# Kernel tuning notes

Hardware: AMD Instinct MI355X
Metric: run time of the kernel (lower is better)

The kernel has to match this reference:

```python
import jax, jax.numpy as jnp
import numpy as np
from math import factorial

N_OBJS = 23

def _f(n):
    return float(factorial(n))

def wigner_d(l, beta):
    """Wigner small-d matrix d^l_{m',m}(beta); shape [2l+1, 2l+1]; m', m in -l..l."""
    mv = np.arange(-l, l + 1)
    cb, sb = np.cos(beta / 2.0), np.sin(beta / 2.0)
    d = np.zeros((2 * l + 1, 2 * l + 1))
    for i, mp in enumerate(mv):
        for j, m in enumerate(mv):
            pref = np.sqrt(_f(l + mp) * _f(l - mp) * _f(l + m) * _f(l - m))
            acc = 0.0
            for s in range(max(0, m - mp), min(l + m, l - mp) + 1):
                acc += ((-1.0) ** (mp - m + s)
                        / (_f(l + m - s) * _f(s) * _f(mp - m + s) * _f(l - mp - s))
                        * cb ** (2 * l + m - mp - 2 * s) * sb ** (mp - m + 2 * s))
            d[i, j] = pref * acc
    return d

def dh_betas(b):
    return np.pi * (2 * np.arange(2 * b) + 1) / (4 * b)

def quad_weights(b):
    """Driscoll-Healy quadrature weights over the 2b beta samples."""
    j = np.arange(2 * b)[:, None]
    k = np.arange(b)[None, :]
    s = (np.sin((2 * j + 1) * (2 * k + 1) * np.pi / (4 * b)) / (2 * k + 1)).sum(1)
    return (2.0 / b) * np.sin(np.pi * (2 * np.arange(2 * b) + 1) / (4 * b)) * s

def s2_fft(x, b_in, nl):
    # x: [N, f, 2b(beta), 2b(alpha)] real -> list over l of [N, f, 2l+1] complex
    xf = jnp.fft.fft(x, axis=-1)
    betas, qw = dh_betas(b_in), quad_weights(b_in)
    out = []
    for l in range(nl):
        dl = np.stack([wigner_d(l, bb)[:, l] for bb in betas])  # [2b, 2l+1] = d^l_{m,0}
        w = jnp.asarray((dl * qw[:, None]).astype(np.complex64))
        idx = np.arange(-l, l + 1) % (2 * b_in)
        out.append(jnp.einsum('nfbm,bm->nfm', xf[..., idx], w))
    return out

def so3_fft(x, b_in, nl):
    # x: [N, f, 2b(beta), 2b(alpha), 2b(gamma)] -> list over l of [N, f, 2l+1, 2l+1]
    xf = jnp.fft.fft2(x, axes=(-2, -1)) / float((2 * b_in) ** 2)
    betas, qw = dh_betas(b_in), quad_weights(b_in)
    out = []
    for l in range(nl):
        d = (np.stack([wigner_d(l, bb) for bb in betas]) * qw[:, None, None]).astype(np.complex64)
        idx = np.arange(-l, l + 1) % (2 * b_in)
        xm = xf[:, :, :, idx[:, None], idx[None, :]]  # [N,f,2b,2l+1,2l+1]
        out.append(jnp.einsum('kmn,afkmn->afmn', jnp.asarray(d), xm))
    return out

def so3_ifft(Z, b):
    # Z: list over l of [N, f, 2l+1, 2l+1] -> real [N, f, 2b, 2b, 2b]
    N, f = Z[0].shape[:2]
    betas = dh_betas(b)
    S = jnp.zeros((N, f, 2 * b, 2 * b, 2 * b), dtype=jnp.complex64)
    for l, Zl in enumerate(Z):
        d = (np.stack([wigner_d(l, bb) for bb in betas]) * (2 * l + 1)).astype(np.complex64)
        T = jnp.einsum('kmn,afmn->afkmn', jnp.asarray(d), Zl)
        idx = np.arange(-l, l + 1) % (2 * b)
        S = S.at[:, :, :, idx[:, None], idx[None, :]].add(T)
    return (jnp.fft.ifft2(S, axes=(-2, -1)) * float((2 * b) ** 2)).real

def s2_rft(kern, nl, alphas, betas):
    # kern: [f_in, f_out, G] real -> list over l of [f_in, f_out, 2l+1] complex
    out = []
    for l in range(nl):
        m = np.arange(-l, l + 1)
        d = np.stack([wigner_d(l, bb)[:, l] for bb in betas])  # [G, 2l+1]
        basis = (d * np.exp(-1j * m[None, :] * alphas[:, None])).astype(np.complex64)
        out.append(jnp.einsum('iog,gm->iom', kern, jnp.asarray(basis)))
    return out

def so3_rft(kern, nl, alphas, betas, gammas):
    out = []
    for l in range(nl):
        m = np.arange(-l, l + 1)
        d = np.stack([wigner_d(l, bb) for bb in betas])  # [G, 2l+1, 2l+1]
        basis = (np.exp(-1j * m[None, :, None] * alphas[:, None, None]) * d
                 * np.exp(-1j * m[None, None, :] * gammas[:, None, None])).astype(np.complex64)
        out.append(jnp.einsum('iog,gmn->iomn', kern, jnp.asarray(basis)))
    return out

def s2_near_identity_grid(n_alpha, n_beta, max_beta=np.pi / 8):
    beta = np.arange(1, n_beta + 1) * max_beta / n_beta
    alpha = np.linspace(0, 2 * np.pi, n_alpha, endpoint=False)
    B, A = np.meshgrid(beta, alpha, indexing='ij')
    return A.ravel(), B.ravel()

def so3_near_identity_grid(n_alpha, n_beta, n_gamma, max_beta=np.pi / 8, max_gamma=np.pi / 8):
    beta = np.arange(1, n_beta + 1) * max_beta / n_beta
    alpha = np.linspace(0, 2 * np.pi, n_alpha, endpoint=False)
    gamma = np.linspace(-max_gamma, max_gamma, n_gamma)
    B, A, G = np.meshgrid(beta, alpha, gamma, indexing='ij')
    return A.ravel(), B.ravel(), G.ravel()

def bn3d(x, w, b, eps=1e-5):
    mu = x.mean(axis=(0, 2, 3, 4), keepdims=True)
    var = x.var(axis=(0, 2, 3, 4), keepdims=True)
    return (x - mu) * jax.lax.rsqrt(var + eps) * w[None, :, None, None, None] + b[None, :, None, None, None]

def bn1d(x, w, b, eps=1e-5):
    mu = x.mean(0)
    var = x.var(0)
    return (x - mu) * jax.lax.rsqrt(var + eps) * w + b

def s2_block(x, kern, bias, bnw, bnb, b_in, b_out):
    X = s2_fft(x, b_in, b_out)
    a, be = s2_near_identity_grid(2 * b_in, 2)
    scale = float(1.0 / np.sqrt(kern.shape[2] * kern.shape[0]))
    Y = s2_rft(kern * scale, b_out, a, be)
    Z = [jnp.einsum('aim,ion->aomn', X[l], jnp.conj(Y[l])) for l in range(b_out)]
    y = so3_ifft(Z, b_out) + bias[None, :, None, None, None]
    return jax.nn.relu(bn3d(y, bnw, bnb))

def so3_block(x, kern, bias, bnw, bnb, b_in, b_out):
    X = so3_fft(x, b_in, b_out)
    a, be, g = so3_near_identity_grid(2 * b_in, 2, 2)
    scale = float(1.0 / np.sqrt(kern.shape[2] * kern.shape[0]))
    Y = so3_rft(kern * scale, b_out, a, be, g)
    Z = [jnp.einsum('aimk,ionk->aomn', X[l], jnp.conj(Y[l])) for l in range(b_out)]
    y = so3_ifft(Z, b_out) + bias[None, :, None, None, None]
    return jax.nn.relu(bn3d(y, bnw, bnb))

def so3_integrate(x):
    b = x.shape[-1] // 2
    w = jnp.asarray(quad_weights(b).astype(np.float32))
    return (x.mean(axis=(-2, -1)) * w).sum(-1)  # weighted beta sum, mean over alpha/gamma

def forward(x, atom_types, k0, c0, g0, d0, k1, c1, g1, d1, k2, c2, g2, d2, k3, c3, g3, d3,
            W1, b1, gw1, gb1, W2, b2, gw2, gb2, W3, b3, gw3, gb3, W4, b4):
    B, n_atoms = x.shape[0], x.shape[1]
    mask = (atom_types > 0).astype(x.dtype)[:, :, None]  # [B, 23, 1]
    h = x.reshape(B * n_atoms, x.shape[2], x.shape[3], x.shape[4])
    h = s2_block(h, k0, c0, g0, d0, 10, 8)
    h = so3_block(h, k1, c1, g1, d1, 8, 6)
    h = so3_block(h, k2, c2, g2, d2, 6, 4)
    h = so3_block(h, k3, c3, g3, d3, 4, 2)
    h = so3_integrate(h)  # [B*23, 64]
    h = jax.nn.relu(bn1d(h @ W1 + b1, gw1, gb1))
    h = jax.nn.relu(bn1d(h @ W2 + b2, gw2, gb2))
    h = (h.reshape(B, N_OBJS, -1) * mask).sum(1)
    h = jax.nn.relu(bn1d(h @ W3 + b3, gw3, gb3))
    return h @ W4 + b4

def setup_inputs():
    key = jax.random.key(0)
    ks = jax.random.split(key, 12)
    B = 64
    return {
        'x': jax.random.normal(ks[0], (B, 23, 5, 20, 20), jnp.float32),
        'atom_types': jax.random.randint(ks[1], (B, 23), 0, 10),
        'k0': jax.random.normal(ks[2], (5, 8, 40), jnp.float32),
        'c0': jnp.zeros((8,), jnp.float32), 'g0': jnp.ones((8,), jnp.float32), 'd0': jnp.zeros((8,), jnp.float32),
        'k1': jax.random.normal(ks[3], (8, 16, 64), jnp.float32),
        'c1': jnp.zeros((16,), jnp.float32), 'g1': jnp.ones((16,), jnp.float32), 'd1': jnp.zeros((16,), jnp.float32),
        'k2': jax.random.normal(ks[4], (16, 32, 48), jnp.float32),
        'c2': jnp.zeros((32,), jnp.float32), 'g2': jnp.ones((32,), jnp.float32), 'd2': jnp.zeros((32,), jnp.float32),
        'k3': jax.random.normal(ks[5], (32, 64, 32), jnp.float32),
        'c3': jnp.zeros((64,), jnp.float32), 'g3': jnp.ones((64,), jnp.float32), 'd3': jnp.zeros((64,), jnp.float32),
        'W1': jax.random.normal(ks[6], (64, 256), jnp.float32) * 0.125,
        'b1': jnp.zeros((256,), jnp.float32), 'gw1': jnp.ones((256,), jnp.float32), 'gb1': jnp.zeros((256,), jnp.float32),
        'W2': jax.random.normal(ks[7], (256, 64), jnp.float32) * 0.0625,
        'b2': jnp.zeros((64,), jnp.float32), 'gw2': jnp.ones((64,), jnp.float32), 'gb2': jnp.zeros((64,), jnp.float32),
        'W3': jax.random.normal(ks[8], (64, 512), jnp.float32) * 0.125,
        'b3': jnp.zeros((512,), jnp.float32), 'gw3': jnp.ones((512,), jnp.float32), 'gb3': jnp.zeros((512,), jnp.float32),
        'W4': jax.random.normal(ks[9], (512, 1), jnp.float32) * 0.044,
        'b4': jnp.zeros((1,), jnp.float32),
    }

def reference(x, atom_types, k0, c0, g0, d0, k1, c1, g1, d1, k2, c2, g2, d2, k3, c3, g3, d3,
              W1, b1, gw1, gb1, W2, b2, gw2, gb2, W3, b3, gw3, gb3, W4, b4):
    return forward(x, atom_types, k0, c0, g0, d0, k1, c1, g1, d1, k2, c2, g2, d2, k3, c3, g3, d3,
                   W1, b1, gw1, gb1, W2, b2, gw2, gb2, W3, b3, gw3, gb3, W4, b4)
```

## Files before the change

kernel.cpp:

```cpp
#include <hip/hip_runtime.h>
#include <cmath>


#define NSAMP 1472
#define PI_D 3.14159265358979323846

constexpr int cBI[4] = {10, 8, 6, 4};
constexpr int cBO[4] = {8, 6, 4, 2};
constexpr int cFI[4] = {5, 8, 16, 32};
constexpr int cFO[4] = {8, 16, 32, 64};
constexpr int cG [4] = {40, 64, 48, 32};
constexpr int cSQ[4] = {680, 286, 84, 10};

__host__ __device__ constexpr int zof(int l) { return (4*l*l*l - l)/3; }

constexpr size_t al64(size_t x){ return (x + 63) & ~(size_t)63; }
constexpr size_t OFS_WF0 = 0;
constexpr size_t OFS_WF1 = al64(OFS_WF0 + 20*64);
constexpr size_t OFS_WF2 = al64(OFS_WF1 + 16*286);
constexpr size_t OFS_WF3 = al64(OFS_WF2 + 12*84);
constexpr size_t OFS_WI0 = al64(OFS_WF3 + 8*10);
constexpr size_t OFS_WI1 = al64(OFS_WI0 + 16*680);
constexpr size_t OFS_WI2 = al64(OFS_WI1 + 12*286);
constexpr size_t OFS_WI3 = al64(OFS_WI2 + 8*84);
// ... 205 lines not shown
            float kv = kr[g];
            float2 b = Bc[bbase + g*w + n];
            re += kv*b.x; im += kv*b.y;
        }
        YC[ybase + t] = make_float2(re, im);
    }
}

__global__ __launch_bounds__(256)
void k_fwd_s2(const float* __restrict__ x, float2* __restrict__ X,
              const float2* __restrict__ Ff, const float* __restrict__ Wf){
    __shared__ float xv[400];
    __shared__ float2 xf[300];
    int tid = threadIdx.x;
    const float* src = x + (size_t)blockIdx.x * 400;
    for (int t = tid; t < 400; t += 256) xv[t] = src[t];
    __syncthreads();
    for (int t = tid; t < 300; t += 256){
        int mi = t % 15, b = t / 15;
        float re = 0.f, im = 0.f;
        for (int al = 0; al < 20; ++al){
            float v = xv[b*20 + al];
            float2 e = Ff[al*15 + mi];
            re += v*e.x; im += v*e.y;
        }
        xf[t] = make_float2(re, im);
    }
    __syncthreads();
    float2* dst = X + (size_t)blockIdx.x * 64;
    int base = 0, lo = 0;
    for (int l = 0; l < 8; ++l){
        int w = 2*l+1;
        for (int t = tid; t < w; t += 256){
            int mi = t - l + 7;
            float re = 0.f, im = 0.f;
            for (int b = 0; b < 20; ++b){
                float wv = Wf[base + b*w + t];
                float2 v = xf[b*15 + mi];
                re += wv*v.x; im += wv*v.y;
            }
            dst[lo + t] = make_float2(re, im);
        }
        base += 20*w; lo += w;
    }
}

template<int T, int L>
__device__ inline float2 mixE(const float2* __restrict__ xs, const float2* __restrict__ Y,
                              int o, int m, int n){
    constexpr int w = 2*L+1;
    constexpr int FI = cFI[T], FO = cFO[T], SQ = cSQ[T];
    float re = 0.f, im = 0.f;
    if constexpr (T == 0){
        const float2* yb = Y + 40*L*L + o*w + n;
        #pragma unroll
        for (int i = 0; i < FI; ++i){
            float2 x = xs[i*64 + L*L + m];
            float2 y = yb[i*8*w];
            re += x.x*y.x - x.y*y.y;
            im += x.x*y.y + x.y*y.x;
        }
    } else {
        const float2* yb = Y + FI*FO*zof(L) + (size_t)o*w + n;
        for (int i = 0; i < FI; ++i){
            const float2* xp = xs + i*SQ + zof(L) + m*w;
            const float2* yp = yb + (size_t)i*w*FO*w;
            #pragma unroll
            for (int k = 0; k < w; ++k){
                float2 x = xp[k];
                float2 y = yp[(size_t)k*FO*w];
                re += x.x*y.x - x.y*y.y;
                im += x.x*y.y + x.y*y.x;
            }
        }
    }
    return make_float2(re, im);
}

template<int T, int OB>
__global__ __launch_bounds__(256)
void k_mix(const float2* __restrict__ Xin, const float2* __restrict__ Y,
           const float* __restrict__ G, const float* __restrict__ hT,
           float2* __restrict__ Z, float2* __restrict__ bnp)
{
    constexpr int FI = cFI[T], FO = cFO[T], NL = cBO[T];
    constexpr int NF = 2*NL-1, OFF = NL-1, SQ = cSQ[T], P = 2*NL;
    constexpr int XPER = (T==0) ? 64 : SQ;
    __shared__ float2 xs[FI*XPER];
    __shared__ float2 zs[OB*SQ];
    const int tid = threadIdx.x;
    constexpr int NOB = FO/OB;
    const int o0 = (blockIdx.x % NOB)*OB;
    const int a  = blockIdx.x / NOB;
    for (int t = tid; t < FI*XPER; t += 256) xs[t] = Xin[(size_t)a*FI*XPER + t];
    __syncthreads();
    float2* Zg = Z + ((size_t)a*FO + o0)*SQ;
    for (int e = tid; e < OB*SQ; e += 256){
        int osub = e / SQ, rem = e % SQ;
        int o = o0 + osub;
        int l = 0, r2 = rem;
        while (r2 >= (2*l+1)*(2*l+1)){ r2 -= (2*l+1)*(2*l+1); ++l; }
        int w = 2*l+1;
        int m = r2 / w, n = r2 % w;
        float2 val = make_float2(0.f, 0.f);
        switch(l){
            case 0: val = mixE<T,0>(xs, Y, o, m, n); break;
            case 1: if constexpr (1 < NL) val = mixE<T,1>(xs, Y, o, m, n); break;
            case 2: if constexpr (2 < NL) val = mixE<T,2>(xs, Y, o, m, n); break;
            case 3: if constexpr (3 < NL) val = mixE<T,3>(xs, Y, o, m, n); break;
            case 4: if constexpr (4 < NL) val = mixE<T,4>(xs, Y, o, m, n); break;
            case 5: if constexpr (5 < NL) val = mixE<T,5>(xs, Y, o, m, n); break;
            case 6: if constexpr (6 < NL) val = mixE<T,6>(xs, Y, o, m, n); break;
            case 7: if constexpr (7 < NL) val = mixE<T,7>(xs, Y, o, m, n); break;
        }
        zs[e] = val;
        Zg[(size_t)osub*SQ + rem] = val;
    }
    __syncthreads();
    const int wave = tid >> 6, lane = tid & 63;
    for (int osub = wave; osub < OB; osub += 4){
        const float2* zp = zs + osub*SQ;
        float pq = 0.f, p0 = 0.f;
        for (int e = lane; e < NF*NF; e += 64){
            int mi = e / NF, ni = e % NF;
            int mm = mi - OFF, nn = ni - OFF;
            int am = mm<0?-mm:mm, an = nn<0?-nn:nn;
            float zr[8], zi[8];
            #pragma unroll
            for (int l = 0; l < NL; ++l){
                bool ok = (l >= am) && (l >= an);
                int idx = ok ? (zof(l) + (mm+l)*(2*l+1) + (nn+l)) : 0;
                float2 zv = zp[idx];
                zr[l] = ok ? zv.x : 0.f;
                zi[l] = ok ? zv.y : 0.f;
            }
            #pragma unroll
            for (int l = 0; l < NL; ++l){
                #pragma unroll
                for (int l2 = 0; l2 < NL; ++l2){
                    float g = G[(l*NL + l2)*NF*NF + e];
                    pq += g*(zr[l]*zr[l2] + zi[l]*zi[l2]);
                }
            }
        }
        if (lane < NL){
            int l = lane;
            p0 = hT[l] * zp[zof(l) + l*(2*l+1) + l].x;
        }
        for (int s = 32; s > 0; s >>= 1){ p0 += __shfl_down(p0, s); pq += __shfl_down(pq, s); }
        if (lane == 0) bnp[(size_t)(o0+osub)*NSAMP + a] = make_float2((float)(P*P)*p0, (float)(P*P)*pq);
    }
}

template<int T, int OB, int CH>
__global__ __launch_bounds__(256)
void k_finv(const float2* __restrict__ Z, const float* __restrict__ Wi, const float2* __restrict__ Fi,
            const float2* __restrict__ Ff, const float* __restrict__ Wf,
            const float* __restrict__ st, const float* __restrict__ gam, const float* __restrict__ bet,
            float2* __restrict__ Xout)
{
    constexpr int FO = cFO[T], NL = cBO[T];
    constexpr int P = 2*NL, NF = 2*NL-1, OFF = NL-1, SQ = cSQ[T];
    constexpr int Tn = T+1;
    constexpr int NLo = cBO[Tn], NFo = 2*NLo-1, OFFo = NLo-1, SQo = cSQ[Tn];
    constexpr float invP2 = 1.0f/(float)(P*P);
    constexpr int szZS = OB*SQ*8;
    constexpr int offS = szZS;
    constexpr int szS  = OB*CH*NF*NF*8;
    constexpr int offT1 = offS + szS;
    constexpr int szT1 = OB*CH*P*NF*8;
    constexpr int szT1B = OB*P*P*NFo*8;
    constexpr int endT1 = offT1 + szT1;
    constexpr int offD = (endT1 > szT1B) ? endT1 : szT1B;
    constexpr int szXV = OB*P*P*P*4;
    constexpr int szSP = OB*P*NFo*NFo*8;
    static_assert(szSP <= szXV, "spec overlay exceeds xv");
    constexpr int LDSZ = offD + szXV;
    __shared__ __align__(16) char smem[LDSZ];
    float2* zs  = (float2*)smem;
    float2* Ssh = (float2*)(smem + offS);
    float2* t1s = (float2*)(smem + offT1);
    float*  xv  = (float*)(smem + offD);

    const int tid = threadIdx.x;
    constexpr int NOB = FO/OB;
    const int o0 = (blockIdx.x % NOB)*OB;
    const int a  = blockIdx.x / NOB;

    for (int t = tid; t < OB*SQ; t += 256) zs[t] = Z[((size_t)a*FO + o0)*SQ + t];
    __syncthreads();

    for (int c0 = 0; c0 < P; c0 += CH){
        for (int t = tid; t < OB*CH*NF*NF; t += 256){
            int ni = t % NF, mi = (t/NF) % NF, kk = (t/(NF*NF)) % CH, osub = t/(NF*NF*CH);
            int k = c0 + kk;
            int mm = mi - OFF, nn = ni - OFF;
            int am = mm < 0 ? -mm : mm, an = nn < 0 ? -nn : nn;
            int l0 = am > an ? am : an;
            const float2* zp = zs + osub*SQ;
            float re = 0.f, im = 0.f;
            int zb = zof(l0);
            for (int l = l0; l < NL; ++l){
                int w = 2*l+1, szl = w*w;
                int rc = (mm + l)*w + (nn + l);
                float wv = Wi[P*zb + k*szl + rc];
                float2 zv = zp[zb + rc];
                re += wv*zv.x; im += wv*zv.y;
                zb += szl;
            }
            Ssh[t] = make_float2(re, im);
        }
        __syncthreads();
        for (int t = tid; t < OB*CH*P*NF; t += 256){
            int ni = t % NF, al = (t/NF) % P, kk = (t/(NF*P)) % CH, osub = t/(NF*P*CH);
            const float2* sb = &Ssh[(osub*CH + kk)*NF*NF];
            float re = 0.f, im = 0.f;
            for (int mi = 0; mi < NF; ++mi){
                float2 s = sb[mi*NF + ni];
                float2 e = Fi[al*NF + mi];
                re += s.x*e.x - s.y*e.y;
                im += s.x*e.y + s.y*e.x;
            }
            t1s[t] = make_float2(re, im);
        }
        __syncthreads();
        for (int t = tid; t < OB*CH*P*P; t += 256){
            int ga = t % P, al = (t/P) % P, kk = (t/(P*P)) % CH, osub = t/(P*P*CH);
            const float2* tb = &t1s[((osub*CH + kk)*P + al)*NF];
            float re = 0.f;
            for (int ni = 0; ni < NF; ++ni){
                float2 v = tb[ni];
                float2 e = Fi[ga*NF + ni];
                re += v.x*e.x - v.y*e.y;
            }
            xv[(osub*P + c0 + kk)*P*P + al*P + ga] = re;
        }
        __syncthreads();
    }

    for (int t = tid; t < OB*P*P*P; t += 256){
        int o = o0 + t/(P*P*P);
        float v = xv[t];
        xv[t] = fmaxf(0.f, (v - st[2*o])*st[2*o+1]*gam[o] + bet[o]);
    }
    __syncthreads();

    float2* t1b = (float2*)smem;
    for (int t = tid; t < OB*P*P*NFo; t += 256){
        int n = t % NFo, kj = (t/NFo) % (P*P), osub = t/(NFo*P*P);
        const float* row = &xv[osub*P*P*P + kj*P];
        float re = 0.f, im = 0.f;
        for (int j = 0; j < P; ++j){
            float v = row[j];
            float2 e = Ff[j*NFo + n];
            re += v*e.x; im += v*e.y;
        }
        t1b[t] = make_float2(re, im);
    }
    __syncthreads();
    float2* spec = (float2*)(smem + offD);
    for (int t = tid; t < OB*P*NFo*NFo; t += 256){
        int n = t % NFo, m = (t/NFo) % NFo, k = (t/(NFo*NFo)) % P, osub = t/(NFo*NFo*P);
        const float2* tb = t1b + osub*P*P*NFo;
        float re = 0.f, im = 0.f;
        for (int j = 0; j < P; ++j){
            float2 v = tb[(k*P + j)*NFo + n];
            float2 e = Ff[j*NFo + m];
            re += v.x*e.x - v.y*e.y;
            im += v.x*e.y + v.y*e.x;
        }
        spec[t] = make_float2(re*invP2, im*invP2);
    }
    __syncthreads();
    for (int t = tid; t < OB*SQo; t += 256){
        int osub = t / SQo, e2 = t % SQo;
        int l = 0, rem = e2;
        while (rem >= (2*l+1)*(2*l+1)){ rem -= (2*l+1)*(2*l+1); ++l; }
        int w = 2*l+1;
        int i2 = rem / w, j2 = rem % w;
        int mi = i2 - l + OFFo, ni = j2 - l + OFFo;
        const float2* sp = spec + osub*P*NFo*NFo;
        float re = 0.f, im = 0.f;
        for (int k = 0; k < P; ++k){
            float wv = Wf[P*zof(l) + k*(w*w) + rem];
            float2 v = sp[(k*NFo + mi)*NFo + ni];
            re += wv*v.x; im += wv*v.y;
        }
        Xout[((size_t)a*FO + o0 + osub)*SQo + e2] = make_float2(re, im);
    }
}

template<int T, int MODE, int OB>
__global__ __launch_bounds__(256)
void k_trans(const float2* __restrict__ Xin, const float2* __restrict__ Y,
             const float* __restrict__ Wi, const float2* __restrict__ Fi,
             const float2* __restrict__ Ff, const float* __restrict__ Wf,
             const float* __restrict__ st, const float* __restrict__ gam, const float* __restrict__ bet,
             float2* __restrict__ Xout, float2* __restrict__ bnp)
{
    constexpr int FI = cFI[T], FO = cFO[T], NL = cBO[T];
    constexpr int P = 2*NL, NF = 2*NL-1, OFF = NL-1, SQ = cSQ[T];
    constexpr int XPER = (T==0) ? 64 : SQ;
    constexpr int Tn = (T < 3) ? T + 1 : 3;
    constexpr int NLo = cBO[Tn], NFo = 2*NLo-1, OFFo = NLo-1, SQo = cSQ[Tn];
    constexpr int CH = (T==0) ? 4 : ((T==1) ? 6 : P);
    constexpr float invP2 = 1.0f/(float)(P*P);

    constexpr int szXS  = FI*XPER*8;
    constexpr int offZS = szXS;
    constexpr int szZS  = OB*SQ*8;
    constexpr int offB  = offZS + szZS;
    constexpr int offS  = offB;
    constexpr int szS   = OB*CH*NF*NF*8;
    constexpr int offT1 = offS + szS;
    constexpr int szT1  = OB*CH*P*NF*8;
    constexpr int offD  = offT1 + szT1;
    constexpr int szXV  = OB*P*P*P*4;
    constexpr int LDSZ = MODE ? (offD + szXV) : (offB + 64);

    __shared__ __align__(16) char smem[LDSZ];
    float2* xs = (float2*)(smem);
    float2* zs = (float2*)(smem + offZS);

    const int tid = threadIdx.x;
    constexpr int NOB = FO/OB;
    const int o0 = (blockIdx.x % NOB) * OB;
    const int a  = blockIdx.x / NOB;

    for (int t = tid; t < FI*XPER; t += 256) xs[t] = Xin[(size_t)a*FI*XPER + t];
    __syncthreads();

    for (int e = tid; e < OB*SQ; e += 256){
        int osub = e / SQ, rem = e % SQ;
        int o = o0 + osub;
        int l = 0;
        while (rem >= (2*l+1)*(2*l+1)){ rem -= (2*l+1)*(2*l+1); ++l; }
        int w = 2*l+1;
        int m = rem / w, n = rem % w;
        float re = 0.f, im = 0.f;
        if constexpr (T == 0){
            const float2* yb = Y + 40*l*l + o*w + n;
            for (int i = 0; i < FI; ++i){
                float2 xv2 = xs[i*64 + l*l + m];
                float2 y = yb[i*8*w];
                re += xv2.x*y.x - xv2.y*y.y;
                im += xv2.x*y.y + xv2.y*y.x;
            }
        } else {
            const float2* yb = Y + FI*FO*zof(l);
            for (int i = 0; i < FI; ++i){
                const float2* xp = &xs[i*SQ + zof(l) + m*w];
                const float2* yp = yb + ((size_t)i*w*FO + o)*w + n;
                for (int k = 0; k < w; ++k){
                    float2 xv2 = xp[k];
                    float2 y = yp[(size_t)k*FO*w];
                    re += xv2.x*y.x - xv2.y*y.y;
                    im += xv2.x*y.y + xv2.y*y.x;
                }
            }
        }
        zs[e] = make_float2(re, im);
    }
    __syncthreads();

    if constexpr (MODE == 0){
        float* wred = (float*)(smem + offB);
        if constexpr (OB == 1){
            float acc0 = 0.f, accQ = 0.f;
            for (int t = tid; t < P*NF*NF; t += 256){
                int ni = t % NF, mi = (t/NF) % NF, k = t/(NF*NF);
                int mm = mi - OFF, nn = ni - OFF;
                int am = mm < 0 ? -mm : mm, an = nn < 0 ? -nn : nn;
                int l0 = am > an ? am : an;
                float re = 0.f, im = 0.f;
                int zb = zof(l0);
                for (int l = l0; l < NL; ++l){
                    int w = 2*l+1, szl = w*w;
                    int rc = (mm + l)*w + (nn + l);
                    float wv = Wi[P*zb + k*szl + rc];
                    float2 zv = zs[zb + rc];
                    re += wv*zv.x; im += wv*zv.y;
                    zb += szl;
                }
                accQ += re*re + im*im;
                if (mm == 0 && nn == 0) acc0 += re;
            }
            for (int s = 32; s > 0; s >>= 1){ acc0 += __shfl_down(acc0, s); accQ += __shfl_down(accQ, s); }
            if ((tid & 63) == 0){ wred[tid>>6] = acc0; wred[4 + (tid>>6)] = accQ; }
            __syncthreads();
            if (tid == 0){
                float a0 = 0.f, a1 = 0.f;
                for (int u = 0; u < 4; ++u){ a0 += wred[u]; a1 += wred[4+u]; }
                bnp[(size_t)o0*NSAMP + a] = make_float2((float)(P*P)*a0, (float)(P*P)*a1);
            }
        } else {
            static_assert(OB == 1 || OB == 4, "stats path expects OB==1 or 4");
            const int wave = tid >> 6, lane = tid & 63;
            const float2* zp = zs + wave*SQ;
            float acc0 = 0.f, accQ = 0.f;
            for (int t = lane; t < P*NF*NF; t += 64){
                int ni = t % NF, mi = (t/NF) % NF, k = t/(NF*NF);
                int mm = mi - OFF, nn = ni - OFF;
                int am = mm < 0 ? -mm : mm, an = nn < 0 ? -nn : nn;
                int l0 = am > an ? am : an;
                float re = 0.f, im = 0.f;
                int zb = zof(l0);
                for (int l = l0; l < NL; ++l){
                    int w = 2*l+1, szl = w*w;
                    int rc = (mm + l)*w + (nn + l);
                    float wv = Wi[P*zb + k*szl + rc];
                    float2 zv = zp[zb + rc];
                    re += wv*zv.x; im += wv*zv.y;
                    zb += szl;
                }
                accQ += re*re + im*im;
                if (mm == 0 && nn == 0) acc0 += re;
            }
            for (int s = 32; s > 0; s >>= 1){ acc0 += __shfl_down(acc0, s); accQ += __shfl_down(accQ, s); }
            if (lane == 0) bnp[(size_t)(o0+wave)*NSAMP + a] = make_float2((float)(P*P)*acc0, (float)(P*P)*accQ);
        }
    } else {
        float2* Ssh = (float2*)(smem + offS);
        float2* t1s = (float2*)(smem + offT1);
        float*  xv  = (float*)(smem + offD);

        for (int c0 = 0; c0 < P; c0 += CH){
            for (int t = tid; t < OB*CH*NF*NF; t += 256){
                int ni = t % NF, mi = (t/NF) % NF, kk = (t/(NF*NF)) % CH, osub = t/(NF*NF*CH);
                int k = c0 + kk;
                int mm = mi - OFF, nn = ni - OFF;
                int am = mm < 0 ? -mm : mm, an = nn < 0 ? -nn : nn;
                int l0 = am > an ? am : an;
                const float2* zp = zs + osub*SQ;
                float re = 0.f, im = 0.f;
                int zb = zof(l0);
                for (int l = l0; l < NL; ++l){
                    int w = 2*l+1, szl = w*w;
                    int rc = (mm + l)*w + (nn + l);
                    float wv = Wi[P*zb + k*szl + rc];
                    float2 zv = zp[zb + rc];
                    re += wv*zv.x; im += wv*zv.y;
// ... 209 lines not shown
    pre1[(size_t)r*256 + tid] = acc;
}

__global__ __launch_bounds__(256)
void k_colstats(const float* __restrict__ x, float* __restrict__ st, int nrow, int ncol){
    int c = blockIdx.x, tid = threadIdx.x;
    double s = 0.0, q = 0.0;
    for (int r = tid; r < nrow; r += 256){
        float v = x[(size_t)r*ncol + c];
        s += v; q += (double)v*(double)v;
    }
    for (int o = 32; o > 0; o >>= 1){ s += __shfl_down(s, o); q += __shfl_down(q, o); }
    __shared__ double rs_[4], rq_[4];
    if ((tid & 63) == 0){ rs_[tid>>6] = s; rq_[tid>>6] = q; }
    __syncthreads();
    if (tid == 0){
        double S = 0.0, Q = 0.0;
        for (int u = 0; u < 4; ++u){ S += rs_[u]; Q += rq_[u]; }
        double mu = S / nrow;
        double var = Q / nrow - mu*mu;
        st[2*c] = (float)mu;
        st[2*c+1] = (float)(1.0 / sqrt(var + 1e-5));
    }
}

__global__ __launch_bounds__(256)
void k_fc2(const float* __restrict__ pre1, const float* __restrict__ st1,
           const float* __restrict__ gw, const float* __restrict__ gb,
           const float* __restrict__ W2, float* __restrict__ pre2){
    __shared__ float hs[256];
    int r = blockIdx.x, tid = threadIdx.x;
    {
        float v = pre1[(size_t)r*256 + tid];
        v = (v - st1[2*tid]) * st1[2*tid+1] * gw[tid] + gb[tid];
        hs[tid] = fmaxf(0.f, v);
    }
    __syncthreads();
    if (tid < 64){
        float acc = 0.f;
        for (int k = 0; k < 256; ++k) acc += hs[k] * W2[k*64 + tid];
        pre2[(size_t)r*64 + tid] = acc;
    }
}

__global__ void k_masksum(const float* __restrict__ pre2, const float* __restrict__ st2,
                          const float* __restrict__ gw, const float* __restrict__ gb,
                          const int* __restrict__ atype, float* __restrict__ sm){
    int b = blockIdx.x, c = threadIdx.x;
    float mu = st2[2*c], rs = st2[2*c+1], g = gw[c], bb = gb[c];
    float acc = 0.f;
    for (int t = 0; t < 23; ++t){
        if (atype[b*23 + t] > 0){
            float v = pre2[((size_t)b*23 + t)*64 + c];
            acc += fmaxf(0.f, (v - mu)*rs*g + bb);
        }
    }
    sm[(size_t)b*64 + c] = acc;
}

__global__ __launch_bounds__(512)
void k_fc3(const float* __restrict__ sm, const float* __restrict__ W3, float* __restrict__ pre3){
    __shared__ float ss[64];
    int b = blockIdx.x, tid = threadIdx.x;
    if (tid < 64) ss[tid] = sm[(size_t)b*64 + tid];
    __syncthreads();
    float acc = 0.f;
    for (int k = 0; k < 64; ++k) acc += ss[k] * W3[k*512 + tid];
    pre3[(size_t)b*512 + tid] = acc;
}

__global__ __launch_bounds__(512)
void k_fc4(const float* __restrict__ pre3, const float* __restrict__ st3,
           const float* __restrict__ gw, const float* __restrict__ gb,
           const float* __restrict__ W4, const float* __restrict__ b4,
           float* __restrict__ out){
    int b = blockIdx.x, tid = threadIdx.x;
    float v = pre3[(size_t)b*512 + tid];
    v = fmaxf(0.f, (v - st3[2*tid]) * st3[2*tid+1] * gw[tid] + gb[tid]);
    float acc = v * W4[tid];
    for (int s = 32; s > 0; s >>= 1) acc += __shfl_down(acc, s);
    __shared__ float wr[8];
    if ((tid & 63) == 0) wr[tid>>6] = acc;
    __syncthreads();
    if (tid == 0){
        float t = 0.f;
        for (int u = 0; u < 8; ++u) t += wr[u];
        out[b] = t + b4[0];
    }
}

extern "C" void kernel_launch(void* const* d_in, const int* in_sizes, int n_in,
                              void* d_out, int out_size, void* d_ws, size_t ws_size,
                              hipStream_t stream){
    (void)in_sizes; (void)n_in; (void)out_size;
    float* ws = (float*)d_ws;
    auto F  = [&](size_t ofs){ return ws + ofs; };
    auto C2 = [&](size_t ofs){ return (float2*)(ws + ofs); };
    const bool bigws = ws_size >= WS_BIG*sizeof(float);

    const float* x    = (const float*)d_in[0];
    const int*  atype = (const int*)d_in[1];
    const float* k0 = (const float*)d_in[2];
    const float* g0 = (const float*)d_in[4];  const float* d0 = (const float*)d_in[5];
    const float* k1 = (const float*)d_in[6];
    const float* g1 = (const float*)d_in[8];  const float* d1 = (const float*)d_in[9];
    const float* k2 = (const float*)d_in[10];
    const float* g2 = (const float*)d_in[12]; const float* d2 = (const float*)d_in[13];
    const float* k3 = (const float*)d_in[14];
    const float* g3 = (const float*)d_in[16]; const float* d3 = (const float*)d_in[17];
    const float* W1 = (const float*)d_in[18];
    const float* gw1 = (const float*)d_in[20]; const float* gb1 = (const float*)d_in[21];
    const float* W2 = (const float*)d_in[22];
    const float* gw2 = (const float*)d_in[24]; const float* gb2 = (const float*)d_in[25];
    const float* W3 = (const float*)d_in[26];
    const float* gw3 = (const float*)d_in[28]; const float* gb3 = (const float*)d_in[29];
    const float* W4 = (const float*)d_in[30]; const float* b4 = (const float*)d_in[31];

    k_init_wf<<<32,256,0,stream>>>(F(OFS_WF0), 10, 8, 1);
    k_init_wf<<<32,256,0,stream>>>(F(OFS_WF1),  8, 6, 0);
    k_init_wf<<<32,256,0,stream>>>(F(OFS_WF2),  6, 4, 0);
    k_init_wf<<<32,256,0,stream>>>(F(OFS_WF3),  4, 2, 0);
    k_init_wi<<<32,256,0,stream>>>(F(OFS_WI0), 8, 8);
    k_init_wi<<<32,256,0,stream>>>(F(OFS_WI1), 6, 6);
    k_init_wi<<<32,256,0,stream>>>(F(OFS_WI2), 4, 4);
    k_init_wi<<<32,256,0,stream>>>(F(OFS_WI3), 2, 2);
    k_init_basis_s2 <<<32,256,0,stream>>>(C2(OFS_BC0), (float)(1.0/sqrt(200.0)));
    k_init_basis_so3<<<64,256,0,stream>>>(C2(OFS_BC1), 16, 6, 64, (float)(1.0/sqrt(512.0)));
    k_init_basis_so3<<<64,256,0,stream>>>(C2(OFS_BC2), 12, 4, 48, (float)(1.0/sqrt(768.0)));
    k_init_basis_so3<<<32,256,0,stream>>>(C2(OFS_BC3),  8, 2, 32, (float)(1.0/32.0));
    k_init_dft<<<2,256,0,stream>>>(C2(OFS_FF0), 20, 15, -1.0);
    k_init_dft<<<2,256,0,stream>>>(C2(OFS_FF1), 16, 11, -1.0);
    k_init_dft<<<2,256,0,stream>>>(C2(OFS_FF2), 12,  7, -1.0);
    k_init_dft<<<2,256,0,stream>>>(C2(OFS_FF3),  8,  3, -1.0);
    k_init_dft<<<2,256,0,stream>>>(C2(OFS_FI0), 16, 15,  1.0);
    k_init_dft<<<2,256,0,stream>>>(C2(OFS_FI1), 12, 11,  1.0);
    k_init_dft<<<2,256,0,stream>>>(C2(OFS_FI2),  8,  7,  1.0);
    k_init_dft<<<2,256,0,stream>>>(C2(OFS_FI3),  4,  3,  1.0);
    k_init_qwi<<<1,64,0,stream>>>(F(OFS_QWI));
    k_mkY_s2<<<dim3(3,8),256,0,stream>>>(C2(OFS_BC0), k0, C2(OFS_YC0));
    k_mkY_so3<1><<<dim3(61,6),256,0,stream>>>(C2(OFS_BC1), k1, C2(OFS_YC1));
    k_mkY_so3<2><<<dim3(98,4),256,0,stream>>>(C2(OFS_BC2), k2, C2(OFS_YC2));
    k_mkY_so3<3><<<dim3(72,2),256,0,stream>>>(C2(OFS_BC3), k3, C2(OFS_YC3));

    k_fwd_s2<<<NSAMP*5,256,0,stream>>>(x, C2(OFS_XA), C2(OFS_FF0), F(OFS_WF0));

    if (bigws){
        k_init_gram<<<32,256,0,stream>>>(F(OFS_WI0), F(OFS_G0), F(OFS_H0), 8);
        k_init_gram<<<32,256,0,stream>>>(F(OFS_WI1), F(OFS_G1), F(OFS_H1), 6);
        k_init_gram<<<32,256,0,stream>>>(F(OFS_WI2), F(OFS_G2), F(OFS_H2), 4);

        k_mix<0,4><<<NSAMP*2,256,0,stream>>>(C2(OFS_XA), C2(OFS_YC0), F(OFS_G0), F(OFS_H0),
                                             C2(OFS_Z), C2(OFS_BNP));
        k_bnred<<<8,256,0,stream>>>(C2(OFS_BNP), F(OFS_BNS), NSAMP, 1.0f/((float)NSAMP*4096.0f));
        k_finv<0,1,4><<<NSAMP*8,256,0,stream>>>(C2(OFS_Z), F(OFS_WI0), C2(OFS_FI0),
                                                C2(OFS_FF1), F(OFS_WF1), F(OFS_BNS), g0, d0, C2(OFS_XB));
        k_mix<1,4><<<NSAMP*4,256,0,stream>>>(C2(OFS_XB), C2(OFS_YC1), F(OFS_G1), F(OFS_H1),
                                             C2(OFS_Z), C2(OFS_BNP));
        k_bnred<<<16,256,0,stream>>>(C2(OFS_BNP), F(OFS_BNS)+128, NSAMP, 1.0f/((float)NSAMP*1728.0f));
        k_finv<1,1,6><<<NSAMP*16,256,0,stream>>>(C2(OFS_Z), F(OFS_WI1), C2(OFS_FI1),
                                                 C2(OFS_FF2), F(OFS_WF2), F(OFS_BNS)+128, g1, d1, C2(OFS_XA));
        k_mix<2,4><<<NSAMP*8,256,0,stream>>>(C2(OFS_XA), C2(OFS_YC2), F(OFS_G2), F(OFS_H2),
                                             C2(OFS_Z), C2(OFS_BNP));
        k_bnred<<<32,256,0,stream>>>(C2(OFS_BNP), F(OFS_BNS)+256, NSAMP, 1.0f/((float)NSAMP*512.0f));
        k_finv<2,2,8><<<NSAMP*16,256,0,stream>>>(C2(OFS_Z), F(OFS_WI2), C2(OFS_FI2),
                                                 C2(OFS_FF3), F(OFS_WF3), F(OFS_BNS)+256, g2, d2, C2(OFS_XB));
    } else {
        k_trans<0,0,1><<<NSAMP*8,256,0,stream>>>(C2(OFS_XA), C2(OFS_YC0), F(OFS_WI0), C2(OFS_FI0),
                                                 nullptr, nullptr, nullptr, nullptr, nullptr,
                                                 nullptr, C2(OFS_BNP));
        k_bnred<<<8,256,0,stream>>>(C2(OFS_BNP), F(OFS_BNS), NSAMP, 1.0f/((float)NSAMP*4096.0f));
        k_trans<0,1,1><<<NSAMP*8,256,0,stream>>>(C2(OFS_XA), C2(OFS_YC0), F(OFS_WI0), C2(OFS_FI0),
                                                 C2(OFS_FF1), F(OFS_WF1), F(OFS_BNS), g0, d0,
                                                 C2(OFS_XB), nullptr);
        k_trans<1,0,1><<<NSAMP*16,256,0,stream>>>(C2(OFS_XB), C2(OFS_YC1), F(OFS_WI1), C2(OFS_FI1),
                                                  nullptr, nullptr, nullptr, nullptr, nullptr,
                                                  nullptr, C2(OFS_BNP));
        k_bnred<<<16,256,0,stream>>>(C2(OFS_BNP), F(OFS_BNS)+128, NSAMP, 1.0f/((float)NSAMP*1728.0f));
        k_trans<1,1,1><<<NSAMP*16,256,0,stream>>>(C2(OFS_XB), C2(OFS_YC1), F(OFS_WI1), C2(OFS_FI1),
                                                  C2(OFS_FF2), F(OFS_WF2), F(OFS_BNS)+128, g1, d1,
                                                  C2(OFS_XA), nullptr);
        k_trans<2,0,4><<<NSAMP*8,256,0,stream>>>(C2(OFS_XA), C2(OFS_YC2), F(OFS_WI2), C2(OFS_FI2),
                                                 nullptr, nullptr, nullptr, nullptr, nullptr,
                                                 nullptr, C2(OFS_BNP));
        k_bnred<<<32,256,0,stream>>>(C2(OFS_BNP), F(OFS_BNS)+256, NSAMP, 1.0f/((float)NSAMP*512.0f));
        k_trans<2,1,4><<<NSAMP*8,256,0,stream>>>(C2(OFS_XA), C2(OFS_YC2), F(OFS_WI2), C2(OFS_FI2),
                                                 C2(OFS_FF3), F(OFS_WF3), F(OFS_BNS)+256, g2, d2,
                                                 C2(OFS_XB), nullptr);
    }

    k_last<0><<<NSAMP,256,0,stream>>>(C2(OFS_XB), C2(OFS_YC3), F(OFS_WI3), C2(OFS_FI3),
                                      nullptr, nullptr, nullptr, nullptr, nullptr, C2(OFS_BNP));
    k_bnred<<<64,256,0,stream>>>(C2(OFS_BNP), F(OFS_BNS)+384, NSAMP, 1.0f/((float)NSAMP*64.0f));
    k_last<1><<<NSAMP,256,0,stream>>>(C2(OFS_XB), C2(OFS_YC3), F(OFS_WI3), C2(OFS_FI3),
                                      F(OFS_BNS)+384, g3, d3, F(OFS_QWI), F(OFS_GOUT), nullptr);

    k_fc1<<<NSAMP,256,0,stream>>>(F(OFS_GOUT), W1, F(OFS_PRE1));
    k_colstats<<<256,256,0,stream>>>(F(OFS_PRE1), F(OFS_ST1), NSAMP, 256);
    k_fc2<<<NSAMP,256,0,stream>>>(F(OFS_PRE1), F(OFS_ST1), gw1, gb1, W2, F(OFS_PRE2));
    k_colstats<<<64,256,0,stream>>>(F(OFS_PRE2), F(OFS_ST2), NSAMP, 64);
    k_masksum<<<64,64,0,stream>>>(F(OFS_PRE2), F(OFS_ST2), gw2, gb2, atype, F(OFS_SM));
    k_fc3<<<64,512,0,stream>>>(F(OFS_SM), W3, F(OFS_PRE3));
    k_colstats<<<512,256,0,stream>>>(F(OFS_PRE3), F(OFS_ST3), 64, 512);
    k_fc4<<<64,512,0,stream>>>(F(OFS_PRE3), F(OFS_ST3), gw3, gb3, W4, b4, (float*)d_out);
}
```

Before: 3.024 ms.

## Stream forward SO3 transform per beta chunk in k_finv to shrink LDS

Restructures k_finv so that each chunk of beta slices runs the inverse transform, BN+ReLU, forward FFT and the partial Wigner contraction together, accumulating the output coefficients in shared memory. The full P^3 volume buffer is no longer held. This cuts LDS footprint, which should raise occupancy and allow more output channels per block; the launch configs change accordingly and inner loops are unrolled. The cost is an extra accumulate pass and more barriers per chunk.

Result: slower. 3.207 ms (+6.1%).

```diff
diff --git a/kernel.cpp b/kernel.cpp
--- a/kernel.cpp
+++ b/kernel.cpp
@@ -381,7 +381,7 @@
     }
 }
 
-template<int T, int OB, int CH>
+template<int T, int OB, int KB>
 __global__ __launch_bounds__(256)
 void k_finv(const float2* __restrict__ Z, const float* __restrict__ Wi, const float2* __restrict__ Fi,
             const float2* __restrict__ Ff, const float* __restrict__ Wf,
@@ -393,23 +393,24 @@
     constexpr int Tn = T+1;
     constexpr int NLo = cBO[Tn], NFo = 2*NLo-1, OFFo = NLo-1, SQo = cSQ[Tn];
     constexpr float invP2 = 1.0f/(float)(P*P);
-    constexpr int szZS = OB*SQ*8;
-    constexpr int offS = szZS;
-    constexpr int szS  = OB*CH*NF*NF*8;
-    constexpr int offT1 = offS + szS;
-    constexpr int szT1 = OB*CH*P*NF*8;
-    constexpr int szT1B = OB*P*P*NFo*8;
-    constexpr int endT1 = offT1 + szT1;
-    constexpr int offD = (endT1 > szT1B) ? endT1 : szT1B;
-    constexpr int szXV = OB*P*P*P*4;
-    constexpr int szSP = OB*P*NFo*NFo*8;
-    static_assert(szSP <= szXV, "spec overlay exceeds xv");
-    constexpr int LDSZ = offD + szXV;
+
+    constexpr int offZS = 0;                 constexpr int szZS = OB*SQ*8;
+    constexpr int offS  = offZS + szZS;      constexpr int szS  = OB*KB*NF*NF*8;
+    constexpr int offT1 = offS + szS;        constexpr int szT1 = OB*KB*P*NF*8;
+    constexpr int offV  = offT1 + szT1;      constexpr int szV  = OB*KB*P*P*4;
+    constexpr int offTB = offV + szV;        constexpr int szTB = OB*KB*P*NFo*8;
+    constexpr int offSP = offTB + szTB;      constexpr int szSP = OB*KB*NFo*NFo*8;
+    constexpr int offXA = offSP + szSP;      constexpr int szXA = OB*SQo*8;
+    constexpr int LDSZ  = offXA + szXA;
+
     __shared__ __align__(16) char smem[LDSZ];
-    float2* zs  = (float2*)smem;
-    float2* Ssh = (float2*)(smem + offS);
-    float2* t1s = (float2*)(smem + offT1);
-    float*  xv  = (float*)(smem + offD);
+    float2* zs   = (float2*)(smem + offZS);
+    float2* Ssh  = (float2*)(smem + offS);
+    float2* t1s  = (float2*)(smem + offT1);
+    float*  vol  = (float*)(smem + offV);
+    float2* t1b  = (float2*)(smem + offTB);
+    float2* spec = (float2*)(smem + offSP);
+    float2* xacc = (float2*)(smem + offXA);
 
     const int tid = threadIdx.x;
     constexpr int NOB = FO/OB;
@@ -417,12 +418,13 @@
     const int a  = blockIdx.x / NOB;
 
     for (int t = tid; t < OB*SQ; t += 256) zs[t] = Z[((size_t)a*FO + o0)*SQ + t];
-    __syncthreads();
-
-    for (int c0 = 0; c0 < P; c0 += CH){
-        for (int t = tid; t < OB*CH*NF*NF; t += 256){
-            int ni = t % NF, mi = (t/NF) % NF, kk = (t/(NF*NF)) % CH, osub = t/(NF*NF*CH);
-            int k = c0 + kk;
+    for (int t = tid; t < OB*SQo; t += 256) xacc[t] = make_float2(0.f, 0.f);
+    __syncthreads();
+
+    for (int k0 = 0; k0 < P; k0 += KB){
+        for (int t = tid; t < OB*KB*NF*NF; t += 256){
+            int ni = t % NF, mi = (t/NF) % NF, kk = (t/(NF*NF)) % KB, osub = t/(NF*NF*KB);
+            int k = k0 + kk;
             int mm = mi - OFF, nn = ni - OFF;
             int am = mm < 0 ? -mm : mm, an = nn < 0 ? -nn : nn;
             int l0 = am > an ? am : an;
@@ -440,10 +442,11 @@
             Ssh[t] = make_float2(re, im);
         }
         __syncthreads();
-        for (int t = tid; t < OB*CH*P*NF; t += 256){
-            int ni = t % NF, al = (t/NF) % P, kk = (t/(NF*P)) % CH, osub = t/(NF*P*CH);
-            const float2* sb = &Ssh[(osub*CH + kk)*NF*NF];
+        for (int t = tid; t < OB*KB*P*NF; t += 256){
+            int ni = t % NF, al = (t/NF) % P, g = t/(NF*P);
+            const float2* sb = &Ssh[g*NF*NF];
             float re = 0.f, im = 0.f;
+            #pragma unroll
             for (int mi = 0; mi < NF; ++mi){
                 float2 s = sb[mi*NF + ni];
                 float2 e = Fi[al*NF + mi];
@@ -453,69 +456,70 @@
             t1s[t] = make_float2(re, im);
         }
         __syncthreads();
-        for (int t = tid; t < OB*CH*P*P; t += 256){
-            int ga = t % P, al = (t/P) % P, kk = (t/(P*P)) % CH, osub = t/(P*P*CH);
-            const float2* tb = &t1s[((osub*CH + kk)*P + al)*NF];
+        for (int t = tid; t < OB*KB*P*P; t += 256){
+            int ga = t % P, al = (t/P) % P, g = t/(P*P);
+            int o = o0 + g/KB;
+            const float2* tb = &t1s[(g*P + al)*NF];
             float re = 0.f;
+            #pragma unroll
             for (int ni = 0; ni < NF; ++ni){
                 float2 v = tb[ni];
                 float2 e = Fi[ga*NF + ni];
                 re += v.x*e.x - v.y*e.y;
             }
-            xv[(osub*P + c0 + kk)*P*P + al*P + ga] = re;
+            vol[t] = fmaxf(0.f, (re - st[2*o])*st[2*o+1]*gam[o] + bet[o]);
         }
         __syncthreads();
-    }
-
-    for (int t = tid; t < OB*P*P*P; t += 256){
-        int o = o0 + t/(P*P*P);
-        float v = xv[t];
-        xv[t] = fmaxf(0.f, (v - st[2*o])*st[2*o+1]*gam[o] + bet[o]);
-    }
-    __syncthreads();
-
-    float2* t1b = (float2*)smem;
-    for (int t = tid; t < OB*P*P*NFo; t += 256){
-        int n = t % NFo, kj = (t/NFo) % (P*P), osub = t/(NFo*P*P);
-        const float* row = &xv[osub*P*P*P + kj*P];
-        float re = 0.f, im = 0.f;
-        for (int j = 0; j < P; ++j){
-            float v = row[j];
-            float2 e = Ff[j*NFo + n];
-            re += v*e.x; im += v*e.y;
-        }
-        t1b[t] = make_float2(re, im);
-    }
-    __syncthreads();
-    float2* spec = (float2*)(smem + offD);
-    for (int t = tid; t < OB*P*NFo*NFo; t += 256){
-        int n = t % NFo, m = (t/NFo) % NFo, k = (t/(NFo*NFo)) % P, osub = t/(NFo*NFo*P);
-        const float2* tb = t1b + osub*P*P*NFo;
-        float re = 0.f, im = 0.f;
-        for (int j = 0; j < P; ++j){
-            float2 v = tb[(k*P + j)*NFo + n];
-            float2 e = Ff[j*NFo + m];
-            re += v.x*e.x - v.y*e.y;
-            im += v.x*e.y + v.y*e.x;
-        }
-        spec[t] = make_float2(re*invP2, im*invP2);
-    }
-    __syncthreads();
+        for (int t = tid; t < OB*KB*P*NFo; t += 256){
+            int n = t % NFo, j1 = (t/NFo) % P, g = t/(NFo*P);
+            const float* row = &vol[(g*P + j1)*P];
+            float re = 0.f, im = 0.f;
+            #pragma unroll
+            for (int j = 0; j < P; ++j){
+                float v = row[j];
+                float2 e = Ff[j*NFo + n];
+                re += v*e.x; im += v*e.y;
+            }
+            t1b[t] = make_float2(re, im);
+        }
+        __syncthreads();
+        for (int t = tid; t < OB*KB*NFo*NFo; t += 256){
+            int n = t % NFo, m = (t/NFo) % NFo, g = t/(NFo*NFo);
+            const float2* tb = &t1b[g*P*NFo];
+            float re = 0.f, im = 0.f;
+            #pragma unroll
+            for (int j = 0; j < P; ++j){
+                float2 v = tb[j*NFo + n];
+                float2 e = Ff[j*NFo + m];
+                re += v.x*e.x - v.y*e.y;
+                im += v.x*e.y + v.y*e.x;
+            }
+            spec[t] = make_float2(re*invP2, im*invP2);
+        }
+        __syncthreads();
+        for (int t = tid; t < OB*SQo; t += 256){
+            int osub = t / SQo, e2 = t % SQo;
+            int l = 0, rem = e2;
+            while (rem >= (2*l+1)*(2*l+1)){ rem -= (2*l+1)*(2*l+1); ++l; }
+            int w = 2*l+1;
+            int i2 = rem / w, j2 = rem % w;
+            int mi = i2 - l + OFFo, ni = j2 - l + OFFo;
+            float re = 0.f, im = 0.f;
+            #pragma unroll
+            for (int kk = 0; kk < KB; ++kk){
+                float wv = Wf[P*zof(l) + (k0+kk)*(w*w) + rem];
+                float2 v = spec[(osub*KB + kk)*NFo*NFo + mi*NFo + ni];
+                re += wv*v.x; im += wv*v.y;
+            }
+            float2 acc = xacc[t];
+            xacc[t] = make_float2(acc.x + re, acc.y + im);
+        }
+        __syncthreads();
+    }
+
     for (int t = tid; t < OB*SQo; t += 256){
         int osub = t / SQo, e2 = t % SQo;
-        int l = 0, rem = e2;
-        while (rem >= (2*l+1)*(2*l+1)){ rem -= (2*l+1)*(2*l+1); ++l; }
-        int w = 2*l+1;
-        int i2 = rem / w, j2 = rem % w;
-        int mi = i2 - l + OFFo, ni = j2 - l + OFFo;
-        const float2* sp = spec + osub*P*NFo*NFo;
-        float re = 0.f, im = 0.f;
-        for (int k = 0; k < P; ++k){
-            float wv = Wf[P*zof(l) + k*(w*w) + rem];
-            float2 v = sp[(k*NFo + mi)*NFo + ni];
-            re += wv*v.x; im += wv*v.y;
-        }
-        Xout[((size_t)a*FO + o0 + osub)*SQo + e2] = make_float2(re, im);
+        Xout[((size_t)a*FO + o0 + osub)*SQo + e2] = xacc[t];
     }
 }
 
@@ -1031,18 +1035,18 @@
         k_mix<0,4><<<NSAMP*2,256,0,stream>>>(C2(OFS_XA), C2(OFS_YC0), F(OFS_G0), F(OFS_H0),
                                              C2(OFS_Z), C2(OFS_BNP));
         k_bnred<<<8,256,0,stream>>>(C2(OFS_BNP), F(OFS_BNS), NSAMP, 1.0f/((float)NSAMP*4096.0f));
-        k_finv<0,1,4><<<NSAMP*8,256,0,stream>>>(C2(OFS_Z), F(OFS_WI0), C2(OFS_FI0),
+        k_finv<0,1,2><<<NSAMP*8,256,0,stream>>>(C2(OFS_Z), F(OFS_WI0), C2(OFS_FI0),
                                                 C2(OFS_FF1), F(OFS_WF1), F(OFS_BNS), g0, d0, C2(OFS_XB));
         k_mix<1,4><<<NSAMP*4,256,0,stream>>>(C2(OFS_XB), C2(OFS_YC1), F(OFS_G1), F(OFS_H1),
                                              C2(OFS_Z), C2(OFS_BNP));
         k_bnred<<<16,256,0,stream>>>(C2(OFS_BNP), F(OFS_BNS)+128, NSAMP, 1.0f/((float)NSAMP*1728.0f));
-        k_finv<1,1,6><<<NSAMP*16,256,0,stream>>>(C2(OFS_Z), F(OFS_WI1), C2(OFS_FI1),
-                                                 C2(OFS_FF2), F(OFS_WF2), F(OFS_BNS)+128, g1, d1, C2(OFS_XA));
+        k_finv<1,2,2><<<NSAMP*8,256,0,stream>>>(C2(OFS_Z), F(OFS_WI1), C2(OFS_FI1),
+                                                C2(OFS_FF2), F(OFS_WF2), F(OFS_BNS)+128, g1, d1, C2(OFS_XA));
         k_mix<2,4><<<NSAMP*8,256,0,stream>>>(C2(OFS_XA), C2(OFS_YC2), F(OFS_G2), F(OFS_H2),
                                              C2(OFS_Z), C2(OFS_BNP));
         k_bnred<<<32,256,0,stream>>>(C2(OFS_BNP), F(OFS_BNS)+256, NSAMP, 1.0f/((float)NSAMP*512.0f));
-        k_finv<2,2,8><<<NSAMP*16,256,0,stream>>>(C2(OFS_Z), F(OFS_WI2), C2(OFS_FI2),
-                                                 C2(OFS_FF3), F(OFS_WF3), F(OFS_BNS)+256, g2, d2, C2(OFS_XB));
+        k_finv<2,4,4><<<NSAMP*8,256,0,stream>>>(C2(OFS_Z), F(OFS_WI2), C2(OFS_FI2),
+                                                C2(OFS_FF3), F(OFS_WF3), F(OFS_BNS)+256, g2, d2, C2(OFS_XB));
     } else {
         k_trans<0,0,1><<<NSAMP*8,256,0,stream>>>(C2(OFS_XA), C2(OFS_YC0), F(OFS_WI0), C2(OFS_FI0),
                                                  nullptr, nullptr, nullptr, nullptr, nullptr,
```
